# Optimization experiments

Hardware: AMD Instinct MI355X
Metric: run time of the kernel (lower is better)

Reference implementation:

```python
import jax, jax.numpy as jnp
import numpy as np

NUM_HEADS = 32
NUM_KV_HEADS = 2
HEAD_DIM = 128
ROTARY_DIM = 64  # partial_rotary_factor 0.5 * head_dim
HIDDEN = 4096
SEQ = 2048


def _rotate_half_interleaved(x):
    # rotates pairs (x0,x1)->(-x1,x0) interleaved, matching torch rotate_half above
    x1 = x[..., 0::2]
    x2 = x[..., 1::2]
    return jnp.stack((-x2, x1), axis=-1).reshape(x.shape)


def _apply_rope(q, k, cos, sin):
    # q: [S, Hq, D], k: [S, Hkv, D], cos/sin: [S, ROTARY_DIM]
    # torch code: take first half of cos/sin then repeat_interleave(2) -> length ROTARY_DIM
    cos_i = jnp.repeat(cos[:, : ROTARY_DIM // 2], 2, axis=-1)[:, None, :]  # [S,1,RD]
    sin_i = jnp.repeat(sin[:, : ROTARY_DIM // 2], 2, axis=-1)[:, None, :]
    q_rot, q_pass = q[..., :ROTARY_DIM], q[..., ROTARY_DIM:]
    k_rot, k_pass = k[..., :ROTARY_DIM], k[..., ROTARY_DIM:]
    q_rot = q_rot * cos_i + _rotate_half_interleaved(q_rot) * sin_i
    k_rot = k_rot * cos_i + _rotate_half_interleaved(k_rot) * sin_i
    return jnp.concatenate([q_rot, q_pass], -1), jnp.concatenate([k_rot, k_pass], -1)


def setup_inputs() -> dict:
    key = jax.random.key(0)
    ks = jax.random.split(key, 6)
    S = SEQ
    qkv_out = (NUM_HEADS + 2 * NUM_KV_HEADS) * HEAD_DIM  # 4608
    hidden_states = jax.random.normal(ks[0], (S, HIDDEN), jnp.float32)
    # realistic rope angles
    inv_freq = 1.0 / (10000.0 ** (np.arange(0, ROTARY_DIM, 2, dtype=np.float32) / ROTARY_DIM))
    ang = np.arange(S, dtype=np.float32)[:, None] * inv_freq[None, :]  # [S, RD/2]
    ang = np.concatenate([ang, ang], axis=-1)  # [S, RD]
    cos = jnp.asarray(np.cos(ang))
    sin = jnp.asarray(np.sin(ang))
    w_qkv = jax.random.normal(ks[1], (HIDDEN, qkv_out), jnp.float32) * 0.02
    b_qkv = jax.random.normal(ks[2], (qkv_out,), jnp.float32) * 0.02
    w_o = jax.random.normal(ks[3], (NUM_HEADS * HEAD_DIM, HIDDEN), jnp.float32) * 0.02
    return {"hidden_states": hidden_states, "cos": cos, "sin": sin,
            "w_qkv": w_qkv, "b_qkv": b_qkv, "w_o": w_o}


def reference(hidden_states, cos, sin, w_qkv, b_qkv, w_o):
    S = hidden_states.shape[0]
    qkv = hidden_states @ w_qkv + b_qkv  # [S, 4608]
    nq = NUM_HEADS * HEAD_DIM
    nkv = NUM_KV_HEADS * HEAD_DIM
    q = qkv[:, :nq].reshape(S, NUM_HEADS, HEAD_DIM)
    k = qkv[:, nq:nq + nkv].reshape(S, NUM_KV_HEADS, HEAD_DIM)
    v = qkv[:, nq + nkv:].reshape(S, NUM_KV_HEADS, HEAD_DIM)
    q, k = _apply_rope(q, k, cos, sin)
    # GQA: repeat kv heads to match q heads
    rep = NUM_HEADS // NUM_KV_HEADS
    k = jnp.repeat(k, rep, axis=1)  # [S, Hq, D]
    v = jnp.repeat(v, rep, axis=1)
    scale = 1.0 / jnp.sqrt(jnp.asarray(HEAD_DIM, q.dtype))
    scores = jnp.einsum("qhd,khd->hqk", q, k) * scale  # [H, S, S]
    causal = jnp.tril(jnp.ones((S, S), bool))
    scores = jnp.where(causal[None], scores, jnp.asarray(-1e30, scores.dtype))
    probs = jax.nn.softmax(scores, axis=-1)
    attn = jnp.einsum("hqk,khd->qhd", probs, v).reshape(S, NUM_HEADS * HEAD_DIM)
    return attn @ w_o  # [S, HIDDEN]
```

## Files before the change

kernel.cpp:

```cpp
#include <hip/hip_runtime.h>
#include <stdint.h>

#define SEQ    2048
#define HIDDEN 4096
#define NQH    32
#define NKVH   2
#define HD     128
#define QKVN   4608
#define ATTN_N 4096

typedef short bf16x8 __attribute__((ext_vector_type(8)));
typedef float f32x4  __attribute__((ext_vector_type(4)));

#define ASYNC16(gp, lp) __builtin_amdgcn_global_load_lds( \
    (const __attribute__((address_space(1))) void*)(gp),  \
    (__attribute__((address_space(3))) void*)(lp), 16, 0, 0)

__device__ __forceinline__ float bf2f(unsigned short u) {
  union { unsigned int i; float f; } v; v.i = ((unsigned int)u) << 16; return v.f;
}
__device__ __forceinline__ unsigned short f2bf(float f) {
  union { float f; unsigned int i; } v; v.f = f;
  unsigned int r = v.i + 0x7fffu + ((v.i >> 16) & 1u);
  return (unsigned short)(r >> 16);
}

__global__ void detect_dtype(const unsigned short* __restrict__ hs, int* __restrict__ flag) {
  int bad = 0;
  for (int i = 0; i < 128; i += 2) {
    const int e = (hs[i] >> 7) & 0xFF;
    if (e < 100 || e > 140) bad++;
  }
  *flag = (bad > 16) ? 1 : 0;
}

__global__ void to_bf16_any(const void* __restrict__ in, unsigned short* __restrict__ out,
                            int n4, const int* __restrict__ flag) {
  const int i = blockIdx.x * blockDim.x + threadIdx.x;
  if (i >= n4) return;
  if (*flag) {
    const float4 f = ((const float4*)in)[i];
    ushort4 u; u.x = f2bf(f.x); u.y = f2bf(f.y); u.z = f2bf(f.z); u.w = f2bf(f.w);
    ((ushort4*)out)[i] = u;
  } else {
    ((ushort4*)out)[i] = ((const ushort4*)in)[i];
  }
}

__global__ void to_f32_any(const void* __restrict__ in, float* __restrict__ out,
                           int n4, const int* __restrict__ flag) {
  const int i = blockIdx.x * blockDim.x + threadIdx.x;
  if (i >= n4) return;
  if (*flag) {
    ((float4*)out)[i] = ((const float4*)in)[i];
  } else {
    const ushort4 u = ((const ushort4*)in)[i];
    float4 f; f.x = bf2f(u.x); f.y = bf2f(u.y); f.z = bf2f(u.z); f.w = bf2f(u.w);
    ((float4*)out)[i] = f;
  }
}

__global__ void transpose_any(const void* __restrict__ in, unsigned short* __restrict__ out,
                              int R, int C, const int* __restrict__ flag) {
  __shared__ unsigned short t[32][36];
  const int r0 = blockIdx.y * 32, c0 = blockIdx.x * 32;
  const int lr = threadIdx.x >> 3;
  const int lc = (threadIdx.x & 7) << 2;
  unsigned short v0, v1, v2, v3;
  if (*flag) {
    const float4 f = *(const float4*)((const float*)in + (size_t)(r0 + lr) * C + c0 + lc);
    v0 = f2bf(f.x); v1 = f2bf(f.y); v2 = f2bf(f.z); v3 = f2bf(f.w);
  } else {
    const ushort4 u = *(const ushort4*)((const unsigned short*)in + (size_t)(r0 + lr) * C + c0 + lc);
    v0 = u.x; v1 = u.y; v2 = u.z; v3 = u.w;
  }
  t[lr][lc] = v0; t[lr][lc + 1] = v1; t[lr][lc + 2] = v2; t[lr][lc + 3] = v3;
  __syncthreads();
  unsigned short* op = out + (size_t)(c0 + lr) * R + r0 + lc;
  ushort4 w;
  w.x = t[lc][lr]; w.y = t[lc + 1][lr]; w.z = t[lc + 2][lr]; w.w = t[lc + 3][lr];
  *(ushort4*)op = w;
}

__global__ __launch_bounds__(256, 2)
void gemm_bt(const unsigned short* __restrict__ A,
             const unsigned short* __restrict__ Bt,
             const float* __restrict__ bias,
             void* __restrict__ C,
             int M, int N, int K, const int* __restrict__ of32) {
  __shared__ __attribute__((aligned(16))) unsigned short As[128 * 32];
  __shared__ __attribute__((aligned(16))) unsigned short Bs[128 * 32];
  const int tid  = threadIdx.x;
  const int wave = tid >> 6, lane = tid & 63;
  const int quad = lane >> 4, l16 = lane & 15;
  const int m0 = blockIdx.y * 128, n0 = blockIdx.x * 128;
  const int wm = (wave >> 1) * 64, wn = (wave & 1) * 64;

  const int crow = tid >> 2;
  const int gsw = ((tid & 3) ^ ((crow >> 1) & 3)) << 3;
  const unsigned short* gA = A + (size_t)(m0 + crow) * K + gsw;
  const unsigned short* gB = Bt + (size_t)(n0 + crow) * K + gsw;
  unsigned short* lA = As + tid * 8;
  unsigned short* lB = Bs + tid * 8;

  const int cxor = (quad ^ ((l16 >> 1) & 3)) << 3;

  f32x4 acc[4][4] = {};

  for (int k0 = 0; k0 < K; k0 += 32) {
    __syncthreads();
    ASYNC16(gA + k0, lA);
    ASYNC16(gA + (size_t)64 * K + k0, lA + 64 * 32);
    ASYNC16(gB + k0, lB);
    ASYNC16(gB + (size_t)64 * K + k0, lB + 64 * 32);
    __syncthreads();
    bf16x8 aF[4], bF[4];
#pragma unroll
    for (int i = 0; i < 4; i++)
      aF[i] = *(const bf16x8*)&As[(wm + i * 16 + l16) * 32 + cxor];
#pragma unroll
    for (int j = 0; j < 4; j++)
      bF[j] = *(const bf16x8*)&Bs[(wn + j * 16 + l16) * 32 + cxor];
#pragma unroll
    for (int i = 0; i < 4; i++)
#pragma unroll
      for (int j = 0; j < 4; j++)
        acc[i][j] = __builtin_amdgcn_mfma_f32_16x16x32_bf16(aF[i], bF[j], acc[i][j], 0, 0, 0);
  }

  const int wf32 = of32 ? *of32 : 0;
#pragma unroll
  for (int j = 0; j < 4; j++) {
    const int col = n0 + wn + j * 16 + l16;
    const float bv = bias ? bias[col] : 0.0f;
#pragma unroll
    for (int i = 0; i < 4; i++) {
#pragma unroll
      for (int r = 0; r < 4; r++) {
        const int row = m0 + wm + i * 16 + quad * 4 + r;
        const float v = acc[i][j][r] + bv;
        const size_t off = (size_t)row * N + col;
        if (wf32) ((float*)C)[off] = v;
        else      ((unsigned short*)C)[off] = f2bf(v);
      }
    }
  }
}

__global__ void rope_split(const unsigned short* __restrict__ qkv,
                           const float* __restrict__ cosb,
                           const float* __restrict__ sinb,
                           unsigned short* __restrict__ qb,
                           unsigned short* __restrict__ kb,
                           unsigned short* __restrict__ vtb) {
  const int s = blockIdx.x;
  const unsigned short* row = qkv + (size_t)s * QKVN;
  const float sc = 0.08838834764831845f * 1.44269504088896341f;
  for (int p = threadIdx.x; p < QKVN / 2; p += blockDim.x) {
    const int col = p << 1;
    const int head = col >> 7;
    const int d = col & 127;
    float x0 = bf2f(row[col]), x1 = bf2f(row[col + 1]);
    float y0 = x0, y1 = x1;
    if (d < 64) {
      const float c  = cosb[s * 64 + (d >> 1)];
      const float sn = sinb[s * 64 + (d >> 1)];
      y0 = x0 * c - x1 * sn;
      y1 = x1 * c + x0 * sn;
    }
    if (head < NQH) {
      const size_t o = (size_t)head * SEQ * HD + (size_t)s * HD + d;
      qb[o] = f2bf(y0 * sc); qb[o + 1] = f2bf(y1 * sc);
    } else if (head < NQH + NKVH) {
      const size_t o = (size_t)(head - NQH) * SEQ * HD + (size_t)s * HD + d;
      kb[o] = f2bf(y0); kb[o + 1] = f2bf(y1);
    } else {
      const size_t o = (size_t)(head - NQH - NKVH) * HD * SEQ + (size_t)d * SEQ + s;
      vtb[o] = f2bf(x0); vtb[o + SEQ] = f2bf(x1);
    }
  }
}

__global__ __launch_bounds__(256, 2)
void attn_fwd(const unsigned short* __restrict__ qb,
              const unsigned short* __restrict__ kb,
              const unsigned short* __restrict__ vtb,
              unsigned short* __restrict__ ob) {
  const int h = blockIdx.x;
  const int qt = 31 - (int)blockIdx.y;
  const int tid = threadIdx.x;
  const int wave = tid >> 6, lane = tid & 63;
  const int quad = lane >> 4, l16 = lane & 15;
  const int q0 = qt * 64 + wave * 16;
  const unsigned short* qh  = qb  + (size_t)h * SEQ * HD;
  const unsigned short* kh  = kb  + (size_t)(h >> 4) * SEQ * HD;
  const unsigned short* vth = vtb + (size_t)(h >> 4) * HD * SEQ;

  __shared__ __attribute__((aligned(16))) unsigned short Ks[2][64 * 128];
  __shared__ __attribute__((aligned(16))) unsigned short Vs[2][128 * 64];
  __shared__ __attribute__((aligned(16))) unsigned short plds[4][16][80];

  bf16x8 qf[4];
#pragma unroll
  for (int kbk = 0; kbk < 4; kbk++)
    qf[kbk] = *(const bf16x8*)&qh[(size_t)(q0 + l16) * HD + kbk * 32 + quad * 8];

  bf16x8 onesf;
#pragma unroll
  for (int i = 0; i < 8; i++) onesf[i] = (short)0x3F80;

  f32x4 oacc[8] = {};
  f32x4 lacc = {};
  float mrow[4] = {-1e30f, -1e30f, -1e30f, -1e30f};

#define STAGEKV(kt_, bsel) do {                                                  \
    const int kb_ = (kt_) * 64;                                                  \
    _Pragma("unroll")                                                            \
    for (int c = 0; c < 4; c++) {                                                \
      const int j = c * 256 + tid;                                               \
      const int key = j >> 4;                                                    \
      const int g = (j & 15) ^ (key & 15);                                       \
      ASYNC16(kh + (size_t)(kb_ + key) * HD + g * 8, &Ks[bsel][0] + j * 8);      \
    }                                                                            \
    _Pragma("unroll")                                                            \
    for (int c = 0; c < 4; c++) {                                                \
      const int j = c * 256 + tid;                                               \
      const int d = j >> 3;                                                      \
      const int g = (j & 7) ^ (d & 7);                                           \
      ASYNC16(vth + (size_t)d * SEQ + kb_ + g * 8, &Vs[bsel][0] + j * 8);        \
    }                                                                            \
  } while (0)

  STAGEKV(0, 0);

  for (int kt = 0; kt <= qt; kt++) {
    const int b = kt & 1;
    const int kbase = kt * 64;
    __syncthreads();
    if (kt < qt) STAGEKV(kt + 1, b ^ 1);

    f32x4 sv[4] = {};
#pragma unroll
    for (int kbk = 0; kbk < 4; kbk++) {
#pragma unroll
      for (int t = 0; t < 4; t++) {
        bf16x8 kf = *(const bf16x8*)&Ks[b][(t * 16 + l16) * 128 + (((kbk << 2) + quad) ^ l16) * 8];
        sv[t] = __builtin_amdgcn_mfma_f32_16x16x32_bf16(qf[kbk], kf, sv[t], 0, 0, 0);
      }
    }
    if (kt == qt) {
#pragma unroll
      for (int t = 0; t < 4; t++) {
        const int key = kbase + t * 16 + l16;
#pragma unroll
        for (int r = 0; r < 4; r++)
          if (key > q0 + quad * 4 + r) sv[t][r] = -1e30f;
      }
    }
    float alpha[4];
#pragma unroll
    for (int r = 0; r < 4; r++) {
      float mx = fmaxf(fmaxf(sv[0][r], sv[1][r]), fmaxf(sv[2][r], sv[3][r]));
#pragma unroll
      for (int off = 8; off; off >>= 1) mx = fmaxf(mx, __shfl_xor(mx, off));
      const float mnew = fmaxf(mrow[r], mx);
      alpha[r] = __builtin_exp2f(mrow[r] - mnew);
      mrow[r] = mnew;
#pragma unroll
      for (int t = 0; t < 4; t++)
        sv[t][r] = __builtin_exp2f(sv[t][r] - mnew);
    }
#pragma unroll
    for (int dt = 0; dt < 8; dt++)
#pragma unroll
      for (int r = 0; r < 4; r++) oacc[dt][r] *= alpha[r];
#pragma unroll
    for (int r = 0; r < 4; r++) lacc[r] *= alpha[r];
#pragma unroll
    for (int r = 0; r < 4; r++)
#pragma unroll
      for (int t = 0; t < 4; t++)
        plds[wave][quad * 4 + r][t * 16 + l16] = f2bf(sv[t][r]);
    bf16x8 pf0 = *(const bf16x8*)&plds[wave][l16][quad * 8];
    bf16x8 pf1 = *(const bf16x8*)&plds[wave][l16][32 + quad * 8];
    lacc = __builtin_amdgcn_mfma_f32_16x16x32_bf16(pf0, onesf, lacc, 0, 0, 0);
    lacc = __builtin_amdgcn_mfma_f32_16x16x32_bf16(pf1, onesf, lacc, 0, 0, 0);
#pragma unroll
    for (int dt = 0; dt < 8; dt++) {
      const int vrow = (dt * 16 + l16) * 64;
      bf16x8 vf0 = *(const bf16x8*)&Vs[b][vrow + ((quad) ^ (l16 & 7)) * 8];
      oacc[dt] = __builtin_amdgcn_mfma_f32_16x16x32_bf16(pf0, vf0, oacc[dt], 0, 0, 0);
      bf16x8 vf1 = *(const bf16x8*)&Vs[b][vrow + ((4 + quad) ^ (l16 & 7)) * 8];
      oacc[dt] = __builtin_amdgcn_mfma_f32_16x16x32_bf16(pf1, vf1, oacc[dt], 0, 0, 0);
    }
  }
#undef STAGEKV
#pragma unroll
  for (int dt = 0; dt < 8; dt++) {
#pragma unroll
    for (int r = 0; r < 4; r++) {
      const float v = oacc[dt][r] / lacc[r];
      ob[(size_t)(q0 + quad * 4 + r) * ATTN_N + h * HD + dt * 16 + l16] = f2bf(v);
    }
  }
}

extern "C" void kernel_launch(void* const* d_in, const int* in_sizes, int n_in,
                              void* d_out, int out_size, void* d_ws, size_t ws_size,
                              hipStream_t stream) {
  const void* hs_raw   = d_in[0];
  const void* cos_raw  = d_in[1];
  const void* sin_raw  = d_in[2];
  const void* wqkv_raw = d_in[3];
  const void* bqkv_raw = d_in[4];
  const void* wo_raw   = d_in[5];
  unsigned short* ws = (unsigned short*)d_ws;

  unsigned short* R1   = ws;
  unsigned short* R2   = R1 + (size_t)QKVN * HIDDEN;
  unsigned short* hs_c = R2 + (size_t)SEQ * QKVN;
  float* cosf  = (float*)(hs_c + (size_t)SEQ * HIDDEN);
  float* sinf  = cosf + SEQ * 64;
  float* biasf = sinf + SEQ * 64;
  int*   flag  = (int*)(biasf + QKVN);

  unsigned short* wt_qkv = R1;
  unsigned short* qbuf   = R1;
  unsigned short* kbuf   = qbuf + (size_t)NQH * SEQ * HD;
  unsigned short* vtbuf  = kbuf + (size_t)NKVH * SEQ * HD;
  unsigned short* wt_o   = R1;
  unsigned short* qkv    = R2;
  unsigned short* attnb  = R2;

  detect_dtype<<<1, 1, 0, stream>>>((const unsigned short*)hs_raw, flag);
  to_bf16_any<<<(SEQ * HIDDEN / 4 + 255) / 256, 256, 0, stream>>>(hs_raw, hs_c, SEQ * HIDDEN / 4, flag);
  to_f32_any<<<(SEQ * 64 / 4 + 255) / 256, 256, 0, stream>>>(cos_raw, cosf, SEQ * 64 / 4, flag);
  to_f32_any<<<(SEQ * 64 / 4 + 255) / 256, 256, 0, stream>>>(sin_raw, sinf, SEQ * 64 / 4, flag);
  to_f32_any<<<(QKVN / 4 + 255) / 256, 256, 0, stream>>>(bqkv_raw, biasf, QKVN / 4, flag);

  transpose_any<<<dim3(QKVN / 32, HIDDEN / 32), 256, 0, stream>>>(wqkv_raw, wt_qkv, HIDDEN, QKVN, flag);
  gemm_bt<<<dim3(QKVN / 128, SEQ / 128), 256, 0, stream>>>(hs_c, wt_qkv, biasf, qkv, SEQ, QKVN, HIDDEN, nullptr);
  rope_split<<<SEQ, 256, 0, stream>>>(qkv, cosf, sinf, qbuf, kbuf, vtbuf);
  attn_fwd<<<dim3(NQH, SEQ / 64), 256, 0, stream>>>(qbuf, kbuf, vtbuf, attnb);
  transpose_any<<<dim3(ATTN_N / 32, HIDDEN / 32), 256, 0, stream>>>(wo_raw, wt_o, HIDDEN, ATTN_N, flag);
  gemm_bt<<<dim3(ATTN_N / 128, SEQ / 128), 256, 0, stream>>>(attnb, wt_o, nullptr, d_out, SEQ, ATTN_N, HIDDEN, flag);
}
```

Baseline: 497.4 us.

## Widen transpose tiles, deepen GEMM K-step, and vectorize rope split

The weight transpose now uses 64x64 tiles, 16-byte vector loads and stores, and writes 8 contiguous output elements per thread. The GEMM stages 64 of K per barrier pair instead of 32 by loading two LDS slabs, which halves the synchronizations and doubles LDS use. rope_split handles 8 elements per thread with vector loads and stores for q and k, and float4 cos/sin loads. These changes target memory-transaction and barrier overhead in the auxiliary kernels and the GEMMs, at the cost of more LDS, which may reduce occupancy.

```diff
diff --git a/kernel.cpp b/kernel.cpp
--- a/kernel.cpp
+++ b/kernel.cpp
@@ -60,26 +60,42 @@
   }
 }
 
-__global__ void transpose_any(const void* __restrict__ in, unsigned short* __restrict__ out,
-                              int R, int C, const int* __restrict__ flag) {
-  __shared__ unsigned short t[32][36];
-  const int r0 = blockIdx.y * 32, c0 = blockIdx.x * 32;
-  const int lr = threadIdx.x >> 3;
-  const int lc = (threadIdx.x & 7) << 2;
-  unsigned short v0, v1, v2, v3;
+__global__ __launch_bounds__(256)
+void transpose64(const void* __restrict__ in, unsigned short* __restrict__ out,
+                 int R, int C, const int* __restrict__ flag) {
+  __shared__ __attribute__((aligned(16))) unsigned short t[64][72];
+  const int r0 = blockIdx.y * 64, c0 = blockIdx.x * 64;
+  const int lr = threadIdx.x >> 2;
+  const int lc = (threadIdx.x & 3) << 4;
+  bf16x8 v0, v1;
   if (*flag) {
-    const float4 f = *(const float4*)((const float*)in + (size_t)(r0 + lr) * C + c0 + lc);
-    v0 = f2bf(f.x); v1 = f2bf(f.y); v2 = f2bf(f.z); v3 = f2bf(f.w);
+    const float* src = (const float*)in + (size_t)(r0 + lr) * C + c0 + lc;
+    const float4 f0 = ((const float4*)src)[0];
+    const float4 f1 = ((const float4*)src)[1];
+    const float4 f2 = ((const float4*)src)[2];
+    const float4 f3 = ((const float4*)src)[3];
+    v0[0] = f2bf(f0.x); v0[1] = f2bf(f0.y); v0[2] = f2bf(f0.z); v0[3] = f2bf(f0.w);
+    v0[4] = f2bf(f1.x); v0[5] = f2bf(f1.y); v0[6] = f2bf(f1.z); v0[7] = f2bf(f1.w);
+    v1[0] = f2bf(f2.x); v1[1] = f2bf(f2.y); v1[2] = f2bf(f2.z); v1[3] = f2bf(f2.w);
+    v1[4] = f2bf(f3.x); v1[5] = f2bf(f3.y); v1[6] = f2bf(f3.z); v1[7] = f2bf(f3.w);
   } else {
-    const ushort4 u = *(const ushort4*)((const unsigned short*)in + (size_t)(r0 + lr) * C + c0 + lc);
-    v0 = u.x; v1 = u.y; v2 = u.z; v3 = u.w;
-  }
-  t[lr][lc] = v0; t[lr][lc + 1] = v1; t[lr][lc + 2] = v2; t[lr][lc + 3] = v3;
+    const unsigned short* src = (const unsigned short*)in + (size_t)(r0 + lr) * C + c0 + lc;
+    v0 = *(const bf16x8*)src;
+    v1 = *(const bf16x8*)(src + 8);
+  }
+  *(bf16x8*)&t[lr][lc]     = v0;
+  *(bf16x8*)&t[lr][lc + 8] = v1;
   __syncthreads();
-  unsigned short* op = out + (size_t)(c0 + lr) * R + r0 + lc;
-  ushort4 w;
-  w.x = t[lc][lr]; w.y = t[lc + 1][lr]; w.z = t[lc + 2][lr]; w.w = t[lc + 3][lr];
-  *(ushort4*)op = w;
+  const int oc = threadIdx.x & 63;
+  const int rb = (threadIdx.x >> 6) * 8;
+#pragma unroll
+  for (int it = 0; it < 2; ++it) {
+    const int rseg = rb + it * 32;
+    bf16x8 w;
+#pragma unroll
+    for (int j = 0; j < 8; j++) w[j] = (short)t[rseg + j][oc];
+    *(bf16x8*)(out + (size_t)(c0 + oc) * R + r0 + rseg) = w;
+  }
 }
 
 __global__ __launch_bounds__(256, 2)
@@ -88,8 +104,8 @@
              const float* __restrict__ bias,
              void* __restrict__ C,
              int M, int N, int K, const int* __restrict__ of32) {
-  __shared__ __attribute__((aligned(16))) unsigned short As[128 * 32];
-  __shared__ __attribute__((aligned(16))) unsigned short Bs[128 * 32];
+  __shared__ __attribute__((aligned(16))) unsigned short As[2][128 * 32];
+  __shared__ __attribute__((aligned(16))) unsigned short Bs[2][128 * 32];
   const int tid  = threadIdx.x;
   const int wave = tid >> 6, lane = tid & 63;
   const int quad = lane >> 4, l16 = lane & 15;
@@ -100,32 +116,39 @@
   const int gsw = ((tid & 3) ^ ((crow >> 1) & 3)) << 3;
   const unsigned short* gA = A + (size_t)(m0 + crow) * K + gsw;
   const unsigned short* gB = Bt + (size_t)(n0 + crow) * K + gsw;
-  unsigned short* lA = As + tid * 8;
-  unsigned short* lB = Bs + tid * 8;
+  const size_t r64 = (size_t)64 * K;
+  const int l8 = tid * 8;
 
   const int cxor = (quad ^ ((l16 >> 1) & 3)) << 3;
 
   f32x4 acc[4][4] = {};
 
-  for (int k0 = 0; k0 < K; k0 += 32) {
+  for (int k0 = 0; k0 < K; k0 += 64) {
     __syncthreads();
-    ASYNC16(gA + k0, lA);
-    ASYNC16(gA + (size_t)64 * K + k0, lA + 64 * 32);
-    ASYNC16(gB + k0, lB);
-    ASYNC16(gB + (size_t)64 * K + k0, lB + 64 * 32);
+    ASYNC16(gA + k0,            &As[0][l8]);
+    ASYNC16(gA + r64 + k0,      &As[0][l8 + 2048]);
+    ASYNC16(gA + k0 + 32,       &As[1][l8]);
+    ASYNC16(gA + r64 + k0 + 32, &As[1][l8 + 2048]);
+    ASYNC16(gB + k0,            &Bs[0][l8]);
+    ASYNC16(gB + r64 + k0,      &Bs[0][l8 + 2048]);
+    ASYNC16(gB + k0 + 32,       &Bs[1][l8]);
+    ASYNC16(gB + r64 + k0 + 32, &Bs[1][l8 + 2048]);
     __syncthreads();
-    bf16x8 aF[4], bF[4];
-#pragma unroll
-    for (int i = 0; i < 4; i++)
-      aF[i] = *(const bf16x8*)&As[(wm + i * 16 + l16) * 32 + cxor];
-#pragma unroll
-    for (int j = 0; j < 4; j++)
-      bF[j] = *(const bf16x8*)&Bs[(wn + j * 16 + l16) * 32 + cxor];
-#pragma unroll
-    for (int i = 0; i < 4; i++)
+#pragma unroll
+    for (int h = 0; h < 2; h++) {
+      bf16x8 aF[4], bF[4];
+#pragma unroll
+      for (int i = 0; i < 4; i++)
+        aF[i] = *(const bf16x8*)&As[h][(wm + i * 16 + l16) * 32 + cxor];
 #pragma unroll
       for (int j = 0; j < 4; j++)
-        acc[i][j] = __builtin_amdgcn_mfma_f32_16x16x32_bf16(aF[i], bF[j], acc[i][j], 0, 0, 0);
+        bF[j] = *(const bf16x8*)&Bs[h][(wn + j * 16 + l16) * 32 + cxor];
+#pragma unroll
+      for (int i = 0; i < 4; i++)
+#pragma unroll
+        for (int j = 0; j < 4; j++)
+          acc[i][j] = __builtin_amdgcn_mfma_f32_16x16x32_bf16(aF[i], bF[j], acc[i][j], 0, 0, 0);
+    }
   }
 
   const int wf32 = of32 ? *of32 : 0;
@@ -156,27 +179,42 @@
   const int s = blockIdx.x;
   const unsigned short* row = qkv + (size_t)s * QKVN;
   const float sc = 0.08838834764831845f * 1.44269504088896341f;
-  for (int p = threadIdx.x; p < QKVN / 2; p += blockDim.x) {
-    const int col = p << 1;
+  for (int p8 = threadIdx.x; p8 < QKVN / 8; p8 += blockDim.x) {
+    const int col = p8 << 3;
     const int head = col >> 7;
     const int d = col & 127;
-    float x0 = bf2f(row[col]), x1 = bf2f(row[col + 1]);
-    float y0 = x0, y1 = x1;
+    const bf16x8 x = *(const bf16x8*)&row[col];
+    if (head >= NQH + NKVH) {
+      const int vh = head - NQH - NKVH;
+      unsigned short* vp = vtb + (size_t)vh * HD * SEQ + (size_t)d * SEQ + s;
+#pragma unroll
+      for (int j = 0; j < 8; j++) vp[(size_t)j * SEQ] = (unsigned short)x[j];
+      continue;
+    }
+    float y[8];
+#pragma unroll
+    for (int j = 0; j < 8; j++) y[j] = bf2f((unsigned short)x[j]);
     if (d < 64) {
-      const float c  = cosb[s * 64 + (d >> 1)];
-      const float sn = sinb[s * 64 + (d >> 1)];
-      y0 = x0 * c - x1 * sn;
-      y1 = x1 * c + x0 * sn;
-    }
+      const float4 c4 = *(const float4*)&cosb[s * 64 + (d >> 1)];
+      const float4 s4 = *(const float4*)&sinb[s * 64 + (d >> 1)];
+      const float cc[4] = {c4.x, c4.y, c4.z, c4.w};
+      const float ss[4] = {s4.x, s4.y, s4.z, s4.w};
+#pragma unroll
+      for (int q = 0; q < 4; q++) {
+        const float x0 = y[2 * q], x1 = y[2 * q + 1];
+        y[2 * q]     = x0 * cc[q] - x1 * ss[q];
+        y[2 * q + 1] = x1 * cc[q] + x0 * ss[q];
+      }
+    }
+    bf16x8 o;
     if (head < NQH) {
-      const size_t o = (size_t)head * SEQ * HD + (size_t)s * HD + d;
-      qb[o] = f2bf(y0 * sc); qb[o + 1] = f2bf(y1 * sc);
-    } else if (head < NQH + NKVH) {
-      const size_t o = (size_t)(head - NQH) * SEQ * HD + (size_t)s * HD + d;
-      kb[o] = f2bf(y0); kb[o + 1] = f2bf(y1);
+#pragma unroll
+      for (int j = 0; j < 8; j++) o[j] = (short)f2bf(y[j] * sc);
+      *(bf16x8*)&qb[(size_t)head * SEQ * HD + (size_t)s * HD + d] = o;
     } else {
-      const size_t o = (size_t)(head - NQH - NKVH) * HD * SEQ + (size_t)d * SEQ + s;
-      vtb[o] = f2bf(x0); vtb[o + SEQ] = f2bf(x1);
+#pragma unroll
+      for (int j = 0; j < 8; j++) o[j] = (short)f2bf(y[j]);
+      *(bf16x8*)&kb[(size_t)(head - NQH) * SEQ * HD + (size_t)s * HD + d] = o;
     }
   }
 }
@@ -338,10 +376,10 @@
   to_f32_any<<<(SEQ * 64 / 4 + 255) / 256, 256, 0, stream>>>(sin_raw, sinf, SEQ * 64 / 4, flag);
   to_f32_any<<<(QKVN / 4 + 255) / 256, 256, 0, stream>>>(bqkv_raw, biasf, QKVN / 4, flag);
 
-  transpose_any<<<dim3(QKVN / 32, HIDDEN / 32), 256, 0, stream>>>(wqkv_raw, wt_qkv, HIDDEN, QKVN, flag);
+  transpose64<<<dim3(QKVN / 64, HIDDEN / 64), 256, 0, stream>>>(wqkv_raw, wt_qkv, HIDDEN, QKVN, flag);
   gemm_bt<<<dim3(QKVN / 128, SEQ / 128), 256, 0, stream>>>(hs_c, wt_qkv, biasf, qkv, SEQ, QKVN, HIDDEN, nullptr);
   rope_split<<<SEQ, 256, 0, stream>>>(qkv, cosf, sinf, qbuf, kbuf, vtbuf);
   attn_fwd<<<dim3(NQH, SEQ / 64), 256, 0, stream>>>(qbuf, kbuf, vtbuf, attnb);
-  transpose_any<<<dim3(ATTN_N / 32, HIDDEN / 32), 256, 0, stream>>>(wo_raw, wt_o, HIDDEN, ATTN_N, flag);
+  transpose64<<<dim3(ATTN_N / 64, HIDDEN / 64), 256, 0, stream>>>(wo_raw, wt_o, HIDDEN, ATTN_N, flag);
   gemm_bt<<<dim3(ATTN_N / 128, SEQ / 128), 256, 0, stream>>>(attnb, wt_o, nullptr, d_out, SEQ, ATTN_N, HIDDEN, flag);
 }
```

Result: no change. 493.9 us (-0.7%).
